# Optimization experiments

Hardware: AMD Instinct MI355X
Metric: run time of the kernel (lower is better)

## Reference

```python
import jax, jax.numpy as jnp
import numpy as np

K = 10
EPS = 1e-5

def leaky(x):
    return jnp.where(x >= 0, x, 0.2 * x)

def graph_feature(x, k):
    # x: (B, C, N) -> edge features (B, 2C, N, k), standard DGCNN get_graph_feature
    B, C, N = x.shape
    xx = jnp.sum(x * x, axis=1)                      # (B, N)
    inner = jnp.einsum('bcn,bcm->bnm', x, x)          # (B, N, N)
    pair = 2.0 * inner - xx[:, :, None] - xx[:, None, :]  # -||xi - xj||^2
    _, idx = jax.lax.top_k(pair, k)                   # (B, N, k)
    xt = jnp.transpose(x, (0, 2, 1))                  # (B, N, C)
    nbr = xt[jnp.arange(B)[:, None, None], idx]       # (B, N, k, C) gather
    ctr = jnp.broadcast_to(xt[:, :, None, :], nbr.shape)
    feat = jnp.concatenate([nbr - ctr, ctr], axis=-1)  # (B, N, k, 2C)
    return jnp.transpose(feat, (0, 3, 1, 2))          # (B, 2C, N, k)

def edge_block(x, W, k):
    # gather -> 1x1 conv (edge MLP) -> leaky relu -> max over neighbors
    e = graph_feature(x, k)                           # (B, 2C, N, k)
    h = leaky(jnp.einsum('oc,bcnk->bonk', W, e))      # (B, O, N, k)
    return jnp.max(h, axis=-1)                        # (B, O, N)

def bn(x, g, b, m, v):
    # inference batchnorm over channel axis 1; x: (B, C, ...) 
    shape = (1, -1) + (1,) * (x.ndim - 2)
    return (x - m.reshape(shape)) * (g.reshape(shape) * jax.lax.rsqrt(v.reshape(shape) + EPS)) + b.reshape(shape)

def setup_inputs() -> dict:
    key = jax.random.key(0)
    ks = jax.random.split(key, 20)
    s = lambda i, shape, scale: (jax.random.normal(ks[i], shape, jnp.float32) * scale)
    inp = {
        'input': jax.random.normal(ks[0], (759, 220, 3), jnp.float32),
        'W1': s(1, (32, 6), 0.4),
        'W2': s(2, (32, 64), 0.15),
        'W3': s(3, (64, 64), 0.15),
        'W4': s(4, (128, 128), 0.1),
        'W5': s(5, (512, 256), 0.08),
        'g5': 1.0 + s(6, (512,), 0.05), 'b5': s(7, (512,), 0.05),
        'm5': s(8, (512,), 0.05), 'v5': 1.0 + 0.1 * jax.random.uniform(ks[9], (512,), jnp.float32),
        'Wl1': s(10, (1024, 1024), 0.03),
        'g6': 1.0 + s(11, (1024,), 0.05), 'b6': s(12, (1024,), 0.05),
        'm6': s(13, (1024,), 0.05), 'v6': 1.0 + 0.1 * jax.random.uniform(ks[14], (1024,), jnp.float32),
        'Wl2': s(15, (380, 1024), 0.03),
        'bl2': s(16, (380,), 0.02),
    }
    return inp

def reference(input, W1, W2, W3, W4, W5, g5, b5, m5, v5, Wl1, g6, b6, m6, v6, Wl2, bl2):
    x = jnp.transpose(input.reshape(-1, 220, 3), (0, 2, 1))  # (B, 3, N)
    x1 = edge_block(x, W1, K)    # (B, 32, N)
    x2 = edge_block(x1, W2, K)   # (B, 32, N)
    x3 = edge_block(x2, W3, K)   # (B, 64, N)
    x4 = edge_block(x3, W4, K)   # (B, 128, N)
    xc = jnp.concatenate([x1, x2, x3, x4], axis=1)           # (B, 256, N)
    h = leaky(bn(jnp.einsum('oc,bcn->bon', W5, xc), g5, b5, m5, v5))  # (B, 512, N)
    p = jnp.concatenate([jnp.max(h, axis=-1), jnp.mean(h, axis=-1)], axis=1)  # (B, 1024)
    z = leaky(bn(p @ Wl1.T, g6, b6, m6, v6))  # dropout is identity in eval
    return z @ Wl2.T + bl2                     # (B, 380)
```

## Files before the change

kernel.cpp:

```cpp
#include <hip/hip_runtime.h>
#include <math.h>

#define NB 759
#define NPT 220
#define KNN 10
#define XCCH 256
#define LDXC (XCCH * NPT)

typedef float f4 __attribute__((ext_vector_type(4)));
typedef float f16v __attribute__((ext_vector_type(16)));
typedef short bf8v __attribute__((ext_vector_type(8)));

__device__ inline unsigned short bfh(float x) {
  unsigned u = __float_as_uint(x);
  unsigned r = u + 0x7FFFu + ((u >> 16) & 1u);
  return (unsigned short)(r >> 16);
}
__device__ inline float bff(unsigned short h) {
  return __uint_as_float(((unsigned)h) << 16);
}
__device__ inline void bfsplit(float x, unsigned short& h, unsigned short& l) {
  h = bfh(x);
  l = bfh(x - bff(h));
}

__global__ __launch_bounds__(256) void k_transpose(const float* __restrict__ in, float* __restrict__ x0) {
  int i = blockIdx.x * 256 + threadIdx.x;
  if (i >= NB * 3 * NPT) return;
  int n = i % NPT; int t = i / NPT; int c = t % 3; int b = t / 3;
  x0[i] = in[(b * NPT + n) * 3 + c];
}

__global__ __launch_bounds__(256) void k_w5split(const float* __restrict__ W5,
    unsigned short* __restrict__ Wh, unsigned short* __restrict__ Wl) {
  int i = blockIdx.x * 256 + threadIdx.x;
  if (i >= 512 * 256) return;
  bfsplit(W5[i], Wh[i], Wl[i]);
}

template<int C>
__global__ __launch_bounds__(256) void k_knn(const float* __restrict__ x, int ldb, int* __restrict__ idxout) {
  constexpr int CP = (C + 4) & ~3;
  __shared__ __align__(16) float xl[NPT * CP];
  __shared__ float xx[NPT];
  int b = blockIdx.x;
  const float* xb = x + (size_t)b * ldb;
  for (int i = threadIdx.x; i < NPT * (CP - C); i += 256) {
    int n = i / (CP - C), c = C + (i % (CP - C));
    xl[n * CP + c] = 0.f;
  }
  for (int i = threadIdx.x; i < C * NPT; i += 256) {
    int c = i / NPT, n = i - c * NPT;
    xl[n * CP + c] = xb[i];
  }
  __syncthreads();
  int n = threadIdx.x;
  f4 xnv[CP / 4];
  float xxn = 0.f;
  if (n < NPT) {
    #pragma unroll
    for (int q = 0; q < CP / 4; ++q) {
      f4 v = *(const f4*)&xl[n * CP + q * 4];
      xnv[q] = v;
      xxn += v.x * v.x; xxn += v.y * v.y; xxn += v.z * v.z; xxn += v.w * v.w;
    }
    xx[n] = xxn;
  }
  __syncthreads();
  if (n >= NPT) return;
  float tv[KNN]; int ti[KNN];
  #pragma unroll
  for (int k = 0; k < KNN; ++k) { tv[k] = -1e30f; ti[k] = 0; }
  for (int m = 0; m < NPT; ++m) {
    float dot = 0.f;
    #pragma unroll
    for (int q = 0; q < CP / 4; ++q) {
      f4 v = *(const f4*)&xl[m * CP + q * 4];
      dot += xnv[q].x * v.x; dot += xnv[q].y * v.y; dot += xnv[q].z * v.z; dot += xnv[q].w * v.w;
    }
    float d = 2.f * dot - xxn - xx[m];
    if (d > tv[KNN - 1]) {
      tv[KNN - 1] = d; ti[KNN - 1] = m;
      #pragma unroll
      for (int j = KNN - 1; j >= 1; --j) {
        if (tv[j] > tv[j - 1]) {
          float tf = tv[j - 1]; tv[j - 1] = tv[j]; tv[j] = tf;
          int tq = ti[j - 1]; ti[j - 1] = ti[j]; ti[j] = tq;
        } else break;
      }
    }
  }
  int* ib = idxout + ((size_t)b * NPT + n) * KNN;
  #pragma unroll
  for (int k = 0; k < KNN; ++k) ib[k] = ti[k];
}

template<int CIN>
__global__ __launch_bounds__(256, 2) void k_conv_fused(const float* __restrict__ x, int ldb,
    const float* __restrict__ W, const int* __restrict__ idxb, float* __restrict__ xout) {
  constexpr int NPAD = 224;
  constexpr int DBS = 224;
  constexpr int REGION = 64 * DBS;
  __shared__ __align__(16) float smem[REGION + CIN * 64];
  __shared__ unsigned short idxl[NPT * KNN];
  float* xl = smem;
  float* db = smem;
  float* wl = smem + REGION;
  int b = blockIdx.x, og = blockIdx.y;
  const float* xb = x + (size_t)b * ldb;
  for (int i = threadIdx.x; i < CIN * NPAD; i += 256) {
    int c = i / NPAD, n = i - c * NPAD;
    xl[i] = (n < NPT) ? xb[c * NPT + n] : 0.f;
  }
  for (int i = threadIdx.x; i < 64 * CIN; i += 256) {
    int rl = i & 63, c = i >> 6;
    int o = og * 32 + (rl & 31);
    float wv = (rl < 32) ? W[o * 2 * CIN + c]
                         : (W[o * 2 * CIN + CIN + c] - W[o * 2 * CIN + c]);
    wl[c * 64 + rl] = wv;
  }
  for (int i = threadIdx.x; i < NPT * KNN; i += 256)
    idxl[i] = (unsigned short)idxb[(size_t)b * NPT * KNN + i];
  __syncthreads();
  int rq = threadIdx.x & 15, nq = threadIdx.x >> 4;
  int gv[4]; bool gok[4];
  #pragma unroll
  for (int j = 0; j < 4; ++j) { int g = nq + j * 16; gok[j] = g < 55; gv[j] = (g < 55 ? g : 54) * 4; }
  f4 acc[4][4];
  #pragma unroll
  for (int j = 0; j < 4; ++j)
    #pragma unroll
    for (int i2 = 0; i2 < 4; ++i2) acc[j][i2] = (f4){0.f, 0.f, 0.f, 0.f};
  #pragma unroll 2
  for (int c = 0; c < CIN; ++c) {
    f4 wv = *(const f4*)&wl[c * 64 + rq * 4];
    #pragma unroll
    for (int j = 0; j < 4; ++j) {
      f4 xv = *(const f4*)&xl[c * NPAD + gv[j]];
      acc[j][0] += wv.x * xv; acc[j][1] += wv.y * xv;
      acc[j][2] += wv.z * xv; acc[j][3] += wv.w * xv;
    }
  }
  __syncthreads();
  #pragma unroll
  for (int j = 0; j < 4; ++j) {
    if (gok[j]) {
      #pragma unroll
      for (int i2 = 0; i2 < 4; ++i2)
        *(f4*)&db[(rq * 4 + i2) * DBS + gv[j]] = acc[j][i2];
    }
  }
  __syncthreads();
  int o0 = og * 32;
  for (int i = threadIdx.x; i < 32 * NPT; i += 256) {
    int ol = i / NPT, n = i - ol * NPT;
    const float* drow = &db[ol * DBS];
    const unsigned short* ib = &idxl[n * KNN];
    float mx = -1e30f;
    #pragma unroll
    for (int k = 0; k < KNN; ++k) mx = fmaxf(mx, drow[ib[k]]);
    float v = mx + db[(32 + ol) * DBS + n];
    xout[((size_t)b * XCCH + o0 + ol) * NPT + n] = (v >= 0.f) ? v : 0.2f * v;
  }
}

#define KP 72
__global__ __launch_bounds__(256) void k_w5_mfma(const float* __restrict__ xc,
    const unsigned short* __restrict__ Wh, const unsigned short* __restrict__ Wl,
    const float* __restrict__ g5, const float* __restrict__ b5, const float* __restrict__ m5,
    const float* __restrict__ v5, float* __restrict__ p) {
  __shared__ __align__(16) unsigned short XH[224 * KP];
  __shared__ __align__(16) unsigned short XL[224 * KP];
  int b = blockIdx.x, rg = blockIdx.y;
  int lane = threadIdx.x & 63, w = threadIdx.x >> 6;
  f16v acc[7];
  #pragma unroll
  for (int t = 0; t < 7; ++t)
    #pragma unroll
    for (int i = 0; i < 16; ++i) acc[t][i] = 0.f;

  int r = rg * 128 + w * 32 + (lane & 31);
  int khalf = (lane >> 5) * 8;

  for (int cb = 0; cb < 4; ++cb) {
    if (cb) __syncthreads();
    for (int i = threadIdx.x; i < 32 * NPT; i += 256) {
      int cp = i / NPT;
      int n = i - cp * NPT;
      int c0 = cp * 2;
      const float* src = &xc[((size_t)b * XCCH + cb * 64 + c0) * NPT + n];
      float x0 = src[0];
      float x1 = src[NPT];
      unsigned short h0, l0, h1, l1;
      bfsplit(x0, h0, l0); bfsplit(x1, h1, l1);
      ((unsigned*)XH)[(n * KP + c0) >> 1] = (unsigned)h0 | ((unsigned)h1 << 16);
      ((unsigned*)XL)[(n * KP + c0) >> 1] = (unsigned)l0 | ((unsigned)l1 << 16);
    }
    for (int i = threadIdx.x; i < 4 * 32; i += 256) {
      int n = NPT + (i >> 5); int cd = i & 31;
      ((unsigned*)XH)[n * (KP / 2) + cd] = 0u;
      ((unsigned*)XL)[n * (KP / 2) + cd] = 0u;
    }
    __syncthreads();
    #pragma unroll
    for (int ks = 0; ks < 4; ++ks) {
      int kg = cb * 64 + ks * 16 + khalf;
      int kl = ks * 16 + khalf;
      bf8v ah = *(const bf8v*)&Wh[(size_t)r * 256 + kg];
      bf8v al = *(const bf8v*)&Wl[(size_t)r * 256 + kg];
      #pragma unroll
      for (int t = 0; t < 7; ++t) {
        int col = t * 32 + (lane & 31);
        bf8v bh = *(const bf8v*)&XH[col * KP + kl];
        bf8v bl = *(const bf8v*)&XL[col * KP + kl];
        acc[t] = __builtin_amdgcn_mfma_f32_32x32x16_bf16(ah, bh, acc[t], 0, 0, 0);
        acc[t] = __builtin_amdgcn_mfma_f32_32x32x16_bf16(al, bh, acc[t], 0, 0, 0);
        acc[t] = __builtin_amdgcn_mfma_f32_32x32x16_bf16(ah, bl, acc[t], 0, 0, 0);
      }
    }
  }
  int rbase = rg * 128 + w * 32 + 4 * (lane >> 5);
  int lc = lane & 31;
  #pragma unroll
  for (int i = 0; i < 16; ++i) {
    int row = rbase + (i & 3) + 8 * (i >> 2);
    float a = g5[row] * rsqrtf(v5[row] + 1e-5f);
    float d = b5[row] - m5[row] * a;
    float mx = -1e30f, sm = 0.f;
    #pragma unroll
    for (int t = 0; t < 7; ++t) {
      bool valid = (t < 6) || (lc < 28);
      float hv = a * acc[t][i] + d;
      float lv = (hv >= 0.f) ? hv : 0.2f * hv;
      if (valid) { mx = fmaxf(mx, lv); sm += lv; }
    }
    #pragma unroll
    for (int m_ = 1; m_ <= 16; m_ <<= 1) {
      mx = fmaxf(mx, __shfl_xor(mx, m_));
      sm += __shfl_xor(sm, m_);
    }
    if (lc == 0) {
      p[(size_t)b * 1024 + row] = mx;
      p[(size_t)b * 1024 + 512 + row] = sm * (1.f / NPT);
    }
  }
}

template<int ON, bool FUSE>
__global__ __launch_bounds__(256) void k_fc(const float* __restrict__ in, const float* __restrict__ Wt,
    const float* __restrict__ q0, const float* __restrict__ q1, const float* __restrict__ q2,
    const float* __restrict__ q3, float* __restrict__ out, int ostride) {
  __shared__ __align__(16) float il[32 * 68];
  __shared__ __align__(16) float wl[32 * 68];
  int b0 = blockIdx.x * 64, o0 = blockIdx.y * 64;
  int oq = threadIdx.x & 15, bq = threadIdx.x >> 4;
  f4 acc[4];
  #pragma unroll
  for (int i2 = 0; i2 < 4; ++i2) acc[i2] = (f4){0.f, 0.f, 0.f, 0.f};
  for (int cb = 0; cb < 32; ++cb) {
    if (cb) __syncthreads();
    for (int i = threadIdx.x; i < 2048; i += 256) {
      int c = i & 31, bb = i >> 5;
      il[c * 68 + bb] = (b0 + bb < NB) ? in[(b0 + bb) * 1024 + cb * 32 + c] : 0.f;
    }
    for (int i = threadIdx.x; i < 2048; i += 256) {
      int c = i & 31, ol = i >> 5;
      wl[c * 68 + ol] = (o0 + ol < ON) ? Wt[(o0 + ol) * 1024 + cb * 32 + c] : 0.f;
    }
    __syncthreads();
    #pragma unroll
    for (int c = 0; c < 32; ++c) {
      f4 wv = *(const f4*)&wl[c * 68 + oq * 4];
      f4 iv = *(const f4*)&il[c * 68 + bq * 4];
      acc[0] += wv.x * iv; acc[1] += wv.y * iv; acc[2] += wv.z * iv; acc[3] += wv.w * iv;
    }
  }
  #pragma unroll
  for (int i2 = 0; i2 < 4; ++i2) {
    int o = o0 + oq * 4 + i2;
    if (o >= ON) continue;
    float A = 1.f, Dv = 0.f;
    if (FUSE) { float a = q0[o] * rsqrtf(q3[o] + 1e-5f); A = a; Dv = q1[o] - q2[o] * a; }
    else { Dv = q0[o]; }
    #pragma unroll
    for (int jj = 0; jj < 4; ++jj) {
      int bb = b0 + bq * 4 + jj;
      if (bb < NB) {
        float v = acc[i2][jj];
        if (FUSE) { v = A * v + Dv; v = (v >= 0.f) ? v : 0.2f * v; }
        else { v = v + Dv; }
        out[(size_t)bb * ostride + o] = v;
      }
    }
  }
}

extern "C" void kernel_launch(void* const* d_in, const int* in_sizes, int n_in,
                              void* d_out, int out_size, void* d_ws, size_t ws_size,
                              hipStream_t stream) {
  const float* input = (const float*)d_in[0];
  const float* W1 = (const float*)d_in[1];
  const float* W2 = (const float*)d_in[2];
  const float* W3 = (const float*)d_in[3];
  const float* W4 = (const float*)d_in[4];
  const float* W5 = (const float*)d_in[5];
  const float* g5 = (const float*)d_in[6];
  const float* b5 = (const float*)d_in[7];
  const float* m5 = (const float*)d_in[8];
  const float* v5 = (const float*)d_in[9];
  const float* Wl1 = (const float*)d_in[10];
  const float* g6 = (const float*)d_in[11];
  const float* b6 = (const float*)d_in[12];
  const float* m6 = (const float*)d_in[13];
  const float* v6 = (const float*)d_in[14];
  const float* Wl2 = (const float*)d_in[15];
  const float* bl2 = (const float*)d_in[16];

  float* w = (float*)d_ws;
  float* x0 = w;
  float* xc = x0 + 500940;
  float* p  = xc + 42746880;
  float* z  = p  + 777216;
  int* idxb = (int*)(z + 777216);
  unsigned short* wh = (unsigned short*)(w + 46472052);
  unsigned short* wlo = wh + 131072;

  k_transpose<<<1957, 256, 0, stream>>>(input, x0);
  k_w5split<<<512, 256, 0, stream>>>(W5, wh, wlo);

  k_knn<3><<<759, 256, 0, stream>>>(x0, 3 * NPT, idxb);
  k_conv_fused<3><<<dim3(759, 1), 256, 0, stream>>>(x0, 3 * NPT, W1, idxb, xc);

  k_knn<32><<<759, 256, 0, stream>>>(xc, LDXC, idxb);
  k_conv_fused<32><<<dim3(759, 1), 256, 0, stream>>>(xc, LDXC, W2, idxb, xc + 32 * NPT);

  k_knn<32><<<759, 256, 0, stream>>>(xc + 32 * NPT, LDXC, idxb);
  k_conv_fused<32><<<dim3(759, 2), 256, 0, stream>>>(xc + 32 * NPT, LDXC, W3, idxb, xc + 64 * NPT);

  k_knn<64><<<759, 256, 0, stream>>>(xc + 64 * NPT, LDXC, idxb);
  k_conv_fused<64><<<dim3(759, 4), 256, 0, stream>>>(xc + 64 * NPT, LDXC, W4, idxb, xc + 128 * NPT);

  k_w5_mfma<<<dim3(759, 4), 256, 0, stream>>>(xc, wh, wlo, g5, b5, m5, v5, p);

  k_fc<1024, true><<<dim3(12, 16), 256, 0, stream>>>(p, Wl1, g6, b6, m6, v6, z, 1024);
  k_fc<380, false><<<dim3(12, 6), 256, 0, stream>>>(z, Wl2, bl2, bl2, bl2, bl2, (float*)d_out, 380);
}
```

Baseline: 1.847 ms.

## Compute two query points per thread in kNN and remap W5 MFMA block order

The kNN kernel now runs 128-thread blocks in which each of 110 active threads handles two query points. Every shared-memory row read of point m is therefore reused for two dot products, halving LDS traffic per distance and giving more independent work per thread. Separately, the W5 MFMA kernel switches to a 1D grid with a swizzled block-to-(batch, row-group) mapping, so that blocks running at the same time share the same batch's xc tile and cache locality improves. Costs include doubled top-k register state, which can lower occupancy, and padded idle blocks in the swizzled grid.

```diff
diff --git a/kernel.cpp b/kernel.cpp
--- a/kernel.cpp
+++ b/kernel.cpp
@@ -38,61 +38,77 @@
   bfsplit(W5[i], Wh[i], Wl[i]);
 }
 
+__device__ inline void topk_insert(float d, int m, float* tv, int* ti) {
+  if (d > tv[KNN - 1]) {
+    tv[KNN - 1] = d; ti[KNN - 1] = m;
+    #pragma unroll
+    for (int j = KNN - 1; j >= 1; --j) {
+      if (tv[j] > tv[j - 1]) {
+        float tf = tv[j - 1]; tv[j - 1] = tv[j]; tv[j] = tf;
+        int tq = ti[j - 1]; ti[j - 1] = ti[j]; ti[j] = tq;
+      } else break;
+    }
+  }
+}
+
 template<int C>
-__global__ __launch_bounds__(256) void k_knn(const float* __restrict__ x, int ldb, int* __restrict__ idxout) {
+__global__ __launch_bounds__(128) void k_knn(const float* __restrict__ x, int ldb, int* __restrict__ idxout) {
   constexpr int CP = (C + 4) & ~3;
   __shared__ __align__(16) float xl[NPT * CP];
   __shared__ float xx[NPT];
   int b = blockIdx.x;
   const float* xb = x + (size_t)b * ldb;
-  for (int i = threadIdx.x; i < NPT * (CP - C); i += 256) {
+  for (int i = threadIdx.x; i < NPT * (CP - C); i += 128) {
     int n = i / (CP - C), c = C + (i % (CP - C));
     xl[n * CP + c] = 0.f;
   }
-  for (int i = threadIdx.x; i < C * NPT; i += 256) {
+  for (int i = threadIdx.x; i < C * NPT; i += 128) {
     int c = i / NPT, n = i - c * NPT;
     xl[n * CP + c] = xb[i];
   }
   __syncthreads();
-  int n = threadIdx.x;
-  f4 xnv[CP / 4];
-  float xxn = 0.f;
-  if (n < NPT) {
+  int t = threadIdx.x;
+  int n0 = t, n1 = t + 110;
+  f4 xra[CP / 4], xrb[CP / 4];
+  float xx0 = 0.f, xx1 = 0.f;
+  if (t < 110) {
     #pragma unroll
     for (int q = 0; q < CP / 4; ++q) {
-      f4 v = *(const f4*)&xl[n * CP + q * 4];
-      xnv[q] = v;
-      xxn += v.x * v.x; xxn += v.y * v.y; xxn += v.z * v.z; xxn += v.w * v.w;
-    }
-    xx[n] = xxn;
-  }
-  __syncthreads();
-  if (n >= NPT) return;
-  float tv[KNN]; int ti[KNN];
-  #pragma unroll
-  for (int k = 0; k < KNN; ++k) { tv[k] = -1e30f; ti[k] = 0; }
+      f4 v = *(const f4*)&xl[n0 * CP + q * 4];
+      xra[q] = v;
+      xx0 += v.x * v.x; xx0 += v.y * v.y; xx0 += v.z * v.z; xx0 += v.w * v.w;
+    }
+    xx[n0] = xx0;
+    #pragma unroll
+    for (int q = 0; q < CP / 4; ++q) {
+      f4 v = *(const f4*)&xl[n1 * CP + q * 4];
+      xrb[q] = v;
+      xx1 += v.x * v.x; xx1 += v.y * v.y; xx1 += v.z * v.z; xx1 += v.w * v.w;
+    }
+    xx[n1] = xx1;
+  }
+  __syncthreads();
+  if (t >= 110) return;
+  float tv0[KNN], tv1[KNN]; int ti0[KNN], ti1[KNN];
+  #pragma unroll
+  for (int k = 0; k < KNN; ++k) { tv0[k] = -1e30f; ti0[k] = 0; tv1[k] = -1e30f; ti1[k] = 0; }
+  #pragma unroll 1
   for (int m = 0; m < NPT; ++m) {
-    float dot = 0.f;
+    float dot0 = 0.f, dot1 = 0.f;
     #pragma unroll
     for (int q = 0; q < CP / 4; ++q) {
       f4 v = *(const f4*)&xl[m * CP + q * 4];
-      dot += xnv[q].x * v.x; dot += xnv[q].y * v.y; dot += xnv[q].z * v.z; dot += xnv[q].w * v.w;
-    }
-    float d = 2.f * dot - xxn - xx[m];
-    if (d > tv[KNN - 1]) {
-      tv[KNN - 1] = d; ti[KNN - 1] = m;
-      #pragma unroll
-      for (int j = KNN - 1; j >= 1; --j) {
-        if (tv[j] > tv[j - 1]) {
-          float tf = tv[j - 1]; tv[j - 1] = tv[j]; tv[j] = tf;
-          int tq = ti[j - 1]; ti[j - 1] = ti[j]; ti[j] = tq;
-        } else break;
-      }
-    }
-  }
-  int* ib = idxout + ((size_t)b * NPT + n) * KNN;
-  #pragma unroll
-  for (int k = 0; k < KNN; ++k) ib[k] = ti[k];
+      dot0 += xra[q].x * v.x; dot0 += xra[q].y * v.y; dot0 += xra[q].z * v.z; dot0 += xra[q].w * v.w;
+      dot1 += xrb[q].x * v.x; dot1 += xrb[q].y * v.y; dot1 += xrb[q].z * v.z; dot1 += xrb[q].w * v.w;
+    }
+    float xxm = xx[m];
+    topk_insert(2.f * dot0 - xx0 - xxm, m, tv0, ti0);
+    topk_insert(2.f * dot1 - xx1 - xxm, m, tv1, ti1);
+  }
+  int* ib0 = idxout + ((size_t)b * NPT + n0) * KNN;
+  int* ib1 = idxout + ((size_t)b * NPT + n1) * KNN;
+  #pragma unroll
+  for (int k = 0; k < KNN; ++k) { ib0[k] = ti0[k]; ib1[k] = ti1[k]; }
 }
 
 template<int CIN>
@@ -171,7 +187,10 @@
     const float* __restrict__ v5, float* __restrict__ p) {
   __shared__ __align__(16) unsigned short XH[224 * KP];
   __shared__ __align__(16) unsigned short XL[224 * KP];
-  int b = blockIdx.x, rg = blockIdx.y;
+  int d = blockIdx.x;
+  int b = (d & 7) * 95 + (d >> 5);
+  int rg = (d >> 3) & 3;
+  if (b >= NB) return;
   int lane = threadIdx.x & 63, w = threadIdx.x >> 6;
   f16v acc[7];
   #pragma unroll
@@ -225,12 +244,12 @@
   for (int i = 0; i < 16; ++i) {
     int row = rbase + (i & 3) + 8 * (i >> 2);
     float a = g5[row] * rsqrtf(v5[row] + 1e-5f);
-    float d = b5[row] - m5[row] * a;
+    float dq = b5[row] - m5[row] * a;
     float mx = -1e30f, sm = 0.f;
     #pragma unroll
     for (int t = 0; t < 7; ++t) {
       bool valid = (t < 6) || (lc < 28);
-      float hv = a * acc[t][i] + d;
+      float hv = a * acc[t][i] + dq;
       float lv = (hv >= 0.f) ? hv : 0.2f * hv;
       if (valid) { mx = fmaxf(mx, lv); sm += lv; }
     }
@@ -328,19 +347,19 @@
   k_transpose<<<1957, 256, 0, stream>>>(input, x0);
   k_w5split<<<512, 256, 0, stream>>>(W5, wh, wlo);
 
-  k_knn<3><<<759, 256, 0, stream>>>(x0, 3 * NPT, idxb);
+  k_knn<3><<<759, 128, 0, stream>>>(x0, 3 * NPT, idxb);
   k_conv_fused<3><<<dim3(759, 1), 256, 0, stream>>>(x0, 3 * NPT, W1, idxb, xc);
 
-  k_knn<32><<<759, 256, 0, stream>>>(xc, LDXC, idxb);
+  k_knn<32><<<759, 128, 0, stream>>>(xc, LDXC, idxb);
   k_conv_fused<32><<<dim3(759, 1), 256, 0, stream>>>(xc, LDXC, W2, idxb, xc + 32 * NPT);
 
-  k_knn<32><<<759, 256, 0, stream>>>(xc + 32 * NPT, LDXC, idxb);
+  k_knn<32><<<759, 128, 0, stream>>>(xc + 32 * NPT, LDXC, idxb);
   k_conv_fused<32><<<dim3(759, 2), 256, 0, stream>>>(xc + 32 * NPT, LDXC, W3, idxb, xc + 64 * NPT);
 
-  k_knn<64><<<759, 256, 0, stream>>>(xc + 64 * NPT, LDXC, idxb);
+  k_knn<64><<<759, 128, 0, stream>>>(xc + 64 * NPT, LDXC, idxb);
   k_conv_fused<64><<<dim3(759, 4), 256, 0, stream>>>(xc + 64 * NPT, LDXC, W4, idxb, xc + 128 * NPT);
 
-  k_w5_mfma<<<dim3(759, 4), 256, 0, stream>>>(xc, wh, wlo, g5, b5, m5, v5, p);
+  k_w5_mfma<<<3040, 256, 0, stream>>>(xc, wh, wlo, g5, b5, m5, v5, p);
 
   k_fc<1024, true><<<dim3(12, 16), 256, 0, stream>>>(p, Wl1, g6, b6, m6, v6, z, 1024);
   k_fc<380, false><<<dim3(12, 6), 256, 0, stream>>>(z, Wl2, bl2, bl2, bl2, bl2, (float*)d_out, 380);
```

After: 2.180 ms. 18.0% more time.

## Compute kNN pairwise distances with split-bf16 MFMA and remap W5 block order

Applied to the files above, without the earlier changes.

For the 32- and 64-channel layers, the kNN kernel now computes the pairwise inner-product matrix with 32x32x16 bf16 MFMA. Each value is split into three bf16 parts and six partial products are summed to recover near-fp32 accuracy. Each wave handles 32 query points, and each lane keeps a partial top-k over half the candidate rows; the two halves are then merged through shared memory. The 3-channel layer gets a simplified scalar kernel, and the W5 GEMM launch becomes a 1D grid with a swizzled batch/row-group mapping, probably to improve cache locality across XCDs. The split-bf16 products may still differ slightly from fp32 and could change neighbor ties.

```diff
diff --git a/kernel.cpp b/kernel.cpp
--- a/kernel.cpp
+++ b/kernel.cpp
@@ -38,61 +38,147 @@
   bfsplit(W5[i], Wh[i], Wl[i]);
 }
 
-template<int C>
-__global__ __launch_bounds__(256) void k_knn(const float* __restrict__ x, int ldb, int* __restrict__ idxout) {
-  constexpr int CP = (C + 4) & ~3;
-  __shared__ __align__(16) float xl[NPT * CP];
+__device__ inline void topk_insert(float d, int m, float* tv, int* ti) {
+  if (d > tv[KNN - 1]) {
+    tv[KNN - 1] = d; ti[KNN - 1] = m;
+    #pragma unroll
+    for (int j = KNN - 1; j >= 1; --j) {
+      if (tv[j] > tv[j - 1]) {
+        float tf = tv[j - 1]; tv[j - 1] = tv[j]; tv[j] = tf;
+        int tq = ti[j - 1]; ti[j - 1] = ti[j]; ti[j] = tq;
+      } else break;
+    }
+  }
+}
+
+__global__ __launch_bounds__(256) void k_knn3(const float* __restrict__ x, int ldb,
+                                              int* __restrict__ idxout) {
+  __shared__ __align__(16) float xl[NPT * 4];
   __shared__ float xx[NPT];
   int b = blockIdx.x;
   const float* xb = x + (size_t)b * ldb;
-  for (int i = threadIdx.x; i < NPT * (CP - C); i += 256) {
-    int n = i / (CP - C), c = C + (i % (CP - C));
-    xl[n * CP + c] = 0.f;
-  }
-  for (int i = threadIdx.x; i < C * NPT; i += 256) {
-    int c = i / NPT, n = i - c * NPT;
-    xl[n * CP + c] = xb[i];
+  for (int i = threadIdx.x; i < NPT; i += 256) {
+    f4 v; v.x = xb[i]; v.y = xb[NPT + i]; v.z = xb[2 * NPT + i]; v.w = 0.f;
+    *(f4*)&xl[i * 4] = v;
+    xx[i] = v.x * v.x + v.y * v.y + v.z * v.z;
   }
   __syncthreads();
   int n = threadIdx.x;
-  f4 xnv[CP / 4];
-  float xxn = 0.f;
-  if (n < NPT) {
-    #pragma unroll
-    for (int q = 0; q < CP / 4; ++q) {
-      f4 v = *(const f4*)&xl[n * CP + q * 4];
-      xnv[q] = v;
-      xxn += v.x * v.x; xxn += v.y * v.y; xxn += v.z * v.z; xxn += v.w * v.w;
-    }
-    xx[n] = xxn;
-  }
-  __syncthreads();
   if (n >= NPT) return;
+  f4 xn = *(const f4*)&xl[n * 4];
+  float xxn = xx[n];
   float tv[KNN]; int ti[KNN];
   #pragma unroll
   for (int k = 0; k < KNN; ++k) { tv[k] = -1e30f; ti[k] = 0; }
   for (int m = 0; m < NPT; ++m) {
-    float dot = 0.f;
-    #pragma unroll
-    for (int q = 0; q < CP / 4; ++q) {
-      f4 v = *(const f4*)&xl[m * CP + q * 4];
-      dot += xnv[q].x * v.x; dot += xnv[q].y * v.y; dot += xnv[q].z * v.z; dot += xnv[q].w * v.w;
-    }
-    float d = 2.f * dot - xxn - xx[m];
-    if (d > tv[KNN - 1]) {
-      tv[KNN - 1] = d; ti[KNN - 1] = m;
-      #pragma unroll
-      for (int j = KNN - 1; j >= 1; --j) {
-        if (tv[j] > tv[j - 1]) {
-          float tf = tv[j - 1]; tv[j - 1] = tv[j]; tv[j] = tf;
-          int tq = ti[j - 1]; ti[j - 1] = ti[j]; ti[j] = tq;
-        } else break;
+    f4 v = *(const f4*)&xl[m * 4];
+    float dot = xn.x * v.x + xn.y * v.y + xn.z * v.z;
+    topk_insert(2.f * dot - xxn - xx[m], m, tv, ti);
+  }
+  int* ib = idxout + ((size_t)b * NPT + n) * KNN;
+  #pragma unroll
+  for (int k = 0; k < KNN; ++k) ib[k] = ti[k];
+}
+
+template<int C>
+__global__ __launch_bounds__(512) void k_knn_mfma(const float* __restrict__ x, int ldb,
+                                                  int* __restrict__ idxout) {
+  constexpr int KPG = C + 8;
+  constexpr int SW = (C / 16) - 1;
+  __shared__ __align__(16) unsigned short XH[224 * KPG];
+  __shared__ __align__(16) unsigned short XM[224 * KPG];
+  __shared__ __align__(16) unsigned short XL[224 * KPG];
+  __shared__ float xx[224];
+  int b = blockIdx.x;
+  const float* xb = x + (size_t)b * ldb;
+  for (int i = threadIdx.x; i < C * 224; i += 512) {
+    int c = i / 224, m = i - c * 224;
+    float v = (m < NPT) ? xb[c * NPT + m] : 0.f;
+    unsigned short h = bfh(v);
+    float r1 = v - bff(h);
+    unsigned short mm = bfh(r1);
+    unsigned short l = bfh(r1 - bff(mm));
+    int cs = c ^ ((m & SW) << 4);
+    XH[m * KPG + cs] = h; XM[m * KPG + cs] = mm; XL[m * KPG + cs] = l;
+  }
+  for (int m = threadIdx.x; m < 224; m += 512) {
+    float s = 0.f;
+    if (m < NPT) {
+      for (int c = 0; c < C; ++c) { float v = xb[c * NPT + m]; s += v * v; }
+    } else s = 1e30f;
+    xx[m] = s;
+  }
+  __syncthreads();
+  int w = threadIdx.x >> 6;
+  int lane = threadIdx.x & 63;
+  int lc = lane & 31, hi = lane >> 5;
+  float tv[KNN]; int ti[KNN];
+  #pragma unroll
+  for (int k = 0; k < KNN; ++k) { tv[k] = -1e30f; ti[k] = 0; }
+  if (w < 7) {
+    int n = w * 32 + lc;
+    f16v acc[7];
+    #pragma unroll
+    for (int mt = 0; mt < 7; ++mt)
+      #pragma unroll
+      for (int i = 0; i < 16; ++i) acc[mt][i] = 0.f;
+    #pragma unroll
+    for (int ks = 0; ks < C / 16; ++ks) {
+      int kb = ks * 16 + hi * 8;
+      int nsw = kb ^ ((n & SW) << 4);
+      bf8v bh = *(const bf8v*)&XH[n * KPG + nsw];
+      bf8v bm = *(const bf8v*)&XM[n * KPG + nsw];
+      bf8v bl = *(const bf8v*)&XL[n * KPG + nsw];
+      #pragma unroll
+      for (int mt = 0; mt < 7; ++mt) {
+        int mr = mt * 32 + lc;
+        int msw = kb ^ ((mr & SW) << 4);
+        bf8v ah = *(const bf8v*)&XH[mr * KPG + msw];
+        bf8v am = *(const bf8v*)&XM[mr * KPG + msw];
+        bf8v al = *(const bf8v*)&XL[mr * KPG + msw];
+        acc[mt] = __builtin_amdgcn_mfma_f32_32x32x16_bf16(ah, bh, acc[mt], 0, 0, 0);
+        acc[mt] = __builtin_amdgcn_mfma_f32_32x32x16_bf16(am, bh, acc[mt], 0, 0, 0);
+        acc[mt] = __builtin_amdgcn_mfma_f32_32x32x16_bf16(ah, bm, acc[mt], 0, 0, 0);
+        acc[mt] = __builtin_amdgcn_mfma_f32_32x32x16_bf16(am, bm, acc[mt], 0, 0, 0);
+        acc[mt] = __builtin_amdgcn_mfma_f32_32x32x16_bf16(al, bh, acc[mt], 0, 0, 0);
+        acc[mt] = __builtin_amdgcn_mfma_f32_32x32x16_bf16(ah, bl, acc[mt], 0, 0, 0);
       }
     }
-  }
-  int* ib = idxout + ((size_t)b * NPT + n) * KNN;
-  #pragma unroll
-  for (int k = 0; k < KNN; ++k) ib[k] = ti[k];
+    float xxn = xx[n];
+    #pragma unroll
+    for (int mt = 0; mt < 7; ++mt)
+      #pragma unroll
+      for (int i = 0; i < 16; ++i) {
+        int m = mt * 32 + (i & 3) + 8 * (i >> 2) + 4 * hi;
+        float d = 2.f * acc[mt][i] - xx[m] - xxn;
+        topk_insert(d, m, tv, ti);
+      }
+  }
+  __syncthreads();
+  float* LV = (float*)XH;
+  int* LI = (int*)XM;
+  if (w < 7) {
+    int slot = (w * 64 + lane) * KNN;
+    #pragma unroll
+    for (int k = 0; k < KNN; ++k) { LV[slot + k] = tv[k]; LI[slot + k] = ti[k]; }
+  }
+  __syncthreads();
+  if (w < 7 && hi == 0) {
+    int n = w * 32 + lc;
+    if (n < NPT) {
+      int sa = (w * 64 + lane) * KNN, sb = sa + 32 * KNN;
+      int a = 0, bq = 0;
+      int* ob = idxout + ((size_t)b * NPT + n) * KNN;
+      #pragma unroll
+      for (int k = 0; k < KNN; ++k) {
+        float va = LV[sa + a], vb = LV[sb + bq];
+        int ia = LI[sa + a], ic = LI[sb + bq];
+        bool ta = (va > vb) || (va == vb && ia < ic);
+        ob[k] = ta ? ia : ic;
+        if (ta) ++a; else ++bq;
+      }
+    }
+  }
 }
 
 template<int CIN>
@@ -171,7 +257,10 @@
     const float* __restrict__ v5, float* __restrict__ p) {
   __shared__ __align__(16) unsigned short XH[224 * KP];
   __shared__ __align__(16) unsigned short XL[224 * KP];
-  int b = blockIdx.x, rg = blockIdx.y;
+  int d = blockIdx.x;
+  int b = (d & 7) * 95 + (d >> 5);
+  int rg = (d >> 3) & 3;
+  if (b >= NB) return;
   int lane = threadIdx.x & 63, w = threadIdx.x >> 6;
   f16v acc[7];
   #pragma unroll
@@ -225,12 +314,12 @@
   for (int i = 0; i < 16; ++i) {
     int row = rbase + (i & 3) + 8 * (i >> 2);
     float a = g5[row] * rsqrtf(v5[row] + 1e-5f);
-    float d = b5[row] - m5[row] * a;
+    float dq = b5[row] - m5[row] * a;
     float mx = -1e30f, sm = 0.f;
     #pragma unroll
     for (int t = 0; t < 7; ++t) {
       bool valid = (t < 6) || (lc < 28);
-      float hv = a * acc[t][i] + d;
+      float hv = a * acc[t][i] + dq;
       float lv = (hv >= 0.f) ? hv : 0.2f * hv;
       if (valid) { mx = fmaxf(mx, lv); sm += lv; }
     }
@@ -328,19 +417,19 @@
   k_transpose<<<1957, 256, 0, stream>>>(input, x0);
   k_w5split<<<512, 256, 0, stream>>>(W5, wh, wlo);
 
-  k_knn<3><<<759, 256, 0, stream>>>(x0, 3 * NPT, idxb);
+  k_knn3<<<759, 256, 0, stream>>>(x0, 3 * NPT, idxb);
   k_conv_fused<3><<<dim3(759, 1), 256, 0, stream>>>(x0, 3 * NPT, W1, idxb, xc);
 
-  k_knn<32><<<759, 256, 0, stream>>>(xc, LDXC, idxb);
+  k_knn_mfma<32><<<759, 512, 0, stream>>>(xc, LDXC, idxb);
   k_conv_fused<32><<<dim3(759, 1), 256, 0, stream>>>(xc, LDXC, W2, idxb, xc + 32 * NPT);
 
-  k_knn<32><<<759, 256, 0, stream>>>(xc + 32 * NPT, LDXC, idxb);
+  k_knn_mfma<32><<<759, 512, 0, stream>>>(xc + 32 * NPT, LDXC, idxb);
   k_conv_fused<32><<<dim3(759, 2), 256, 0, stream>>>(xc + 32 * NPT, LDXC, W3, idxb, xc + 64 * NPT);
 
-  k_knn<64><<<759, 256, 0, stream>>>(xc + 64 * NPT, LDXC, idxb);
+  k_knn_mfma<64><<<759, 512, 0, stream>>>(xc + 64 * NPT, LDXC, idxb);
   k_conv_fused<64><<<dim3(759, 4), 256, 0, stream>>>(xc + 64 * NPT, LDXC, W4, idxb, xc + 128 * NPT);
 
-  k_w5_mfma<<<dim3(759, 4), 256, 0, stream>>>(xc, wh, wlo, g5, b5, m5, v5, p);
+  k_w5_mfma<<<3040, 256, 0, stream>>>(xc, wh, wlo, g5, b5, m5, v5, p);
 
   k_fc<1024, true><<<dim3(12, 16), 256, 0, stream>>>(p, Wl1, g6, b6, m6, v6, z, 1024);
   k_fc<380, false><<<dim3(12, 6), 256, 0, stream>>>(z, Wl2, bl2, bl2, bl2, bl2, (float*)d_out, 380);
```

New measurement: 1.698 ms. 1.09x faster.
